# Kernel tuning notes

Measured on AMD Instinct MI355X. Metric: run time of the kernel, lower is better.

The kernel has to match this reference:

```python
import jax, jax.numpy as jnp
import numpy as np

N_NODES = 100000
N_EDGES = 800000
IN_FEATS = 128
OUT_FEATS = 128
RANK_DIM = 128
NUM_BOND_TYPES = 32


def setup_inputs() -> dict:
    key = jax.random.key(0)
    ks = jax.random.split(key, 8)
    feat = jax.random.normal(ks[0], (N_NODES, IN_FEATS), dtype=jnp.float32)
    src = jax.random.randint(ks[1], (N_EDGES,), 0, N_NODES)
    dst = jax.random.randint(ks[2], (N_EDGES,), 0, N_NODES)
    # guarantee every node has in-degree >= 1 (module forbids 0-in-degree nodes)
    dst = dst.at[:N_NODES].set(jnp.arange(N_NODES))
    edge_attr = jax.random.randint(ks[3], (N_EDGES,), 0, NUM_BOND_TYPES)
    # xavier-uniform-like params
    def xavier(k, shape):
        lim = float(np.sqrt(6.0 / (shape[0] + shape[1])))
        return jax.random.uniform(k, shape, jnp.float32, -lim, lim)
    w1 = xavier(ks[4], (IN_FEATS, OUT_FEATS))
    w2 = xavier(ks[5], (IN_FEATS + 1, RANK_DIM))
    v = xavier(ks[6], (RANK_DIM, OUT_FEATS))
    bond_emb = jax.random.normal(ks[7], (NUM_BOND_TYPES, OUT_FEATS), dtype=jnp.float32)
    return {"feat": feat, "src": src, "dst": dst, "edge_attr": edge_attr,
            "w1": w1, "w2": w2, "v": v, "bond_emb": bond_emb}


def reference(feat, src, dst, edge_attr, w1, w2, v, bond_emb):
    N = feat.shape[0]
    E = src.shape[0]
    ones_e = jnp.ones((E,), dtype=feat.dtype)
    # norm == 'both': scale source features by out_degree^{-1/2}
    out_deg = jnp.clip(jax.ops.segment_sum(ones_e, src, num_segments=N), 1.0)
    feat_src = feat * (out_deg ** -0.5)[:, None]
    # two small GEMMs on node features
    h_sum = feat_src @ w1  # [N, out]
    feat_aug = jnp.concatenate([feat_src, jnp.ones((N, 1), dtype=feat.dtype)], axis=1)
    h_prod = jnp.tanh(feat_aug @ w2)  # [N, rank]
    # edge embedding (BondEncoder)
    ew = bond_emb[edge_attr]  # [E, out]
    # u_mul_e then neighbor-wise product / sum reductions onto dst
    m_prod = h_prod[src] * ew
    m_sum = h_sum[src] * ew
    hp = jax.ops.segment_prod(m_prod, dst, num_segments=N)
    hs = jax.ops.segment_sum(m_sum, dst, num_segments=N)
    rst = hs + hp @ v
    # norm == 'both': scale result by in_degree^{-1/2}
    in_deg = jnp.clip(jax.ops.segment_sum(ones_e, dst, num_segments=N), 1.0)
    rst = rst * (in_deg ** -0.5)[:, None]
    return rst
```

## Files before the change

### kernel.cpp

```cpp
#include <hip/hip_runtime.h>

#define N_NODES 100000
#define N_EDGES 800000

typedef unsigned short u16;
typedef unsigned int u32;
typedef __attribute__((ext_vector_type(8))) short short8;
typedef __attribute__((ext_vector_type(4))) float floatx4;

#define NBUK 196
#define BSH 9
#define NBLK 512
#define NE4 (N_EDGES / 4)
#define CE 391
#define NB_PREPW 192

__device__ __forceinline__ float bflo(u32 u) {
    union { u32 i; float f; } v; v.i = u << 16; return v.f;
}
__device__ __forceinline__ float bfhi(u32 u) {
    union { u32 i; float f; } v; v.i = u & 0xFFFF0000u; return v.f;
}
__device__ __forceinline__ u16 f2bf(float f) {
    union { float f; u32 i; } v; v.f = f;
    u32 r = (v.i + 0x7FFFu + ((v.i >> 16) & 1u)) >> 16;
    return (u16)r;
}
__device__ __forceinline__ float fast_tanh(float x) {
    float e = __expf(2.0f * x);
    return 1.0f - 2.0f * __builtin_amdgcn_rcpf(e + 1.0f);
}


__global__ __launch_bounds__(256) void kA_count(const int* __restrict__ src, const int* __restrict__ dst,
                                                int* __restrict__ countsD, int* __restrict__ countsS,
                                                const float* __restrict__ w1, const float* __restrict__ w2,
                                                const float* __restrict__ v, u16* __restrict__ wvfrag) {
    __shared__ int cd[NBUK], cs[NBUK];
    if (blockIdx.x >= NBLK) {
        int idx = (blockIdx.x - NBLK) * 256 + threadIdx.x;
        if (idx < 3 * 16384) {
            int m = idx >> 14, r = idx & 16383;
            int k = r >> 7, o = r & 127;
            float val = (m == 0) ? w1[k * 128 + o] : (m == 1) ? w2[k * 128 + o] : v[k * 128 + o];
            int ot = o >> 4, ks = k >> 5, quad = (k >> 3) & 3, j = k & 7;
            int lane = (quad << 4) | (o & 15);
            wvfrag[(((m * 8 + ot) * 4 + ks) * 64 + lane) * 8 + j] = f2bf(val);
        }
        return;
    }
    for (int i = threadIdx.x; i < NBUK; i += 256) { cd[i] = 0; cs[i] = 0; }
    __syncthreads();
    int i0 = blockIdx.x * CE;
    int i1 = i0 + CE; if (i1 > NE4) i1 = NE4;
    for (int i = i0 + threadIdx.x; i < i1; i += 256) {
        int4 d4 = ((const int4*)dst)[i];
        int4 s4 = ((const int4*)src)[i];
        atomicAdd(&cd[d4.x >> BSH], 1); atomicAdd(&cd[d4.y >> BSH], 1);
        atomicAdd(&cd[d4.z >> BSH], 1); atomicAdd(&cd[d4.w >> BSH], 1);
        atomicAdd(&cs[s4.x >> BSH], 1); atomicAdd(&cs[s4.y >> BSH], 1);
        atomicAdd(&cs[s4.z >> BSH], 1); atomicAdd(&cs[s4.w >> BSH], 1);
    }
    __syncthreads();
    for (int i = threadIdx.x; i < NBUK; i += 256) {
        countsD[i * NBLK + blockIdx.x] = cd[i];
        countsS[i * NBLK + blockIdx.x] = cs[i];
    }
}


__global__ __launch_bounds__(256) void kA_scan(int* __restrict__ countsD, int* __restrict__ countsS,
                                               int* __restrict__ totD, int* __restrict__ totS) {
    __shared__ int sc[256];
    int b = blockIdx.x;
    int* cnt = (b < NBUK) ? (countsD + b * NBLK) : (countsS + (b - NBUK) * NBLK);
    int t = threadIdx.x;
    int v0 = cnt[2 * t], v1 = cnt[2 * t + 1];
    int s = v0 + v1;
    sc[t] = s; __syncthreads();
    for (int off = 1; off < 256; off <<= 1) {
        int x = (t >= off) ? sc[t - off] : 0;
        __syncthreads();
        sc[t] += x;
        __syncthreads();
    }
    int excl = sc[t] - s;
    cnt[2 * t] = excl; cnt[2 * t + 1] = excl + v0;
    if (t == 255) { if (b < NBUK) totD[b] = sc[255]; else totS[b - NBUK] = sc[255]; }
}


__global__ __launch_bounds__(256) void kA_scatter(const int* __restrict__ src, const int* __restrict__ dst,
                                                  const int* __restrict__ attr,
                                                  const int* __restrict__ countsD, const int* __restrict__ countsS,
                                                  const int* __restrict__ totD, const int* __restrict__ totS,
                                                  uint2* __restrict__ dbuf, int* __restrict__ sbuf) {
    __shared__ int curD[NBUK], curS[NBUK];
    __shared__ int sd[256], ss[256];
    int t = threadIdx.x;
    int vd = (t < NBUK) ? totD[t] : 0;
    int vs = (t < NBUK) ? totS[t] : 0;
    sd[t] = vd; ss[t] = vs; __syncthreads();
    for (int off = 1; off < 256; off <<= 1) {
        int xd = (t >= off) ? sd[t - off] : 0;
        int xs = (t >= off) ? ss[t - off] : 0;
        __syncthreads();
        sd[t] += xd; ss[t] += xs;
        __syncthreads();
    }
    if (t < NBUK) {
        curD[t] = (sd[t] - vd) + countsD[t * NBLK + blockIdx.x];
        curS[t] = (ss[t] - vs) + countsS[t * NBLK + blockIdx.x];
    }
    __syncthreads();
    int i0 = blockIdx.x * CE;
    int i1 = i0 + CE; if (i1 > NE4) i1 = NE4;
    for (int i = i0 + t; i < i1; i += 256) {
        int4 s4 = ((const int4*)src)[i];
        int4 d4 = ((const int4*)dst)[i];
        int4 a4 = ((const int4*)attr)[i];
        int p, d, s, a;
        d = d4.x; s = s4.x; a = a4.x;
        p = atomicAdd(&curD[d >> BSH], 1); dbuf[p] = make_uint2((u32)d, (u32)((s << 5) | a));
        p = atomicAdd(&curS[s >> BSH], 1); sbuf[p] = s;
        d = d4.y; s = s4.y; a = a4.y;
        p = atomicAdd(&curD[d >> BSH], 1); dbuf[p] = make_uint2((u32)d, (u32)((s << 5) | a));
        p = atomicAdd(&curS[s >> BSH], 1); sbuf[p] = s;
        d = d4.z; s = s4.z; a = a4.z;
        p = atomicAdd(&curD[d >> BSH], 1); dbuf[p] = make_uint2((u32)d, (u32)((s << 5) | a));
        p = atomicAdd(&curS[s >> BSH], 1); sbuf[p] = s;
        d = d4.w; s = s4.w; a = a4.w;
        p = atomicAdd(&curD[d >> BSH], 1); dbuf[p] = make_uint2((u32)d, (u32)((s << 5) | a));
        p = atomicAdd(&curS[s >> BSH], 1); sbuf[p] = s;
    }
}


__global__ __launch_bounds__(256) void k_build(const uint2* __restrict__ dbuf, const int* __restrict__ sbuf,
                                               const int* __restrict__ totD, const int* __restrict__ totS,
                                               int* __restrict__ csr_start, int* __restrict__ in_deg,
                                               float* __restrict__ in_scale, float* __restrict__ out_scale,
                                               int* __restrict__ csr_edge) {
    __shared__ int cnt[512];
    __shared__ int aux[512];
    __shared__ int sc[256];
    __shared__ int sbase;
    int t = threadIdx.x;
    int isS = blockIdx.x >= NBUK;
    int b = isS ? (blockIdx.x - NBUK) : blockIdx.x;
    const int* tot = isS ? totS : totD;
    if (t < 64) {
        int s = 0;
        for (int i = t; i < b; i += 64) s += tot[i];
#pragma unroll
        for (int o = 32; o > 0; o >>= 1) s += __shfl_down(s, o);
        if (t == 0) sbase = s;
    }
    for (int i = t; i < 512; i += 256) cnt[i] = 0;
    __syncthreads();
    int st = sbase, n = tot[b];
    int nb0 = b << BSH;
    if (isS) {
        for (int i = st + t; i < st + n; i += 256) atomicAdd(&cnt[sbuf[i] - nb0], 1);
        __syncthreads();
        for (int s2 = t; s2 < 512; s2 += 256) {
            int node = nb0 + s2;
            if (node < N_NODES) { int c = cnt[s2]; if (c < 1) c = 1; out_scale[node] = rsqrtf((float)c); }
        }
        return;
    }
    for (int i = st + t; i < st + n; i += 256) { uint2 r = dbuf[i]; atomicAdd(&cnt[(int)r.x - nb0], 1); }
    __syncthreads();
    int c0 = cnt[2 * t], c1 = cnt[2 * t + 1];
    int s = c0 + c1; sc[t] = s; __syncthreads();
    for (int off = 1; off < 256; off <<= 1) {
        int x = (t >= off) ? sc[t - off] : 0;
        __syncthreads();
        sc[t] += x;
        __syncthreads();
    }
    int excl = sc[t] - s;
    aux[2 * t] = excl; aux[2 * t + 1] = excl + c0;
    int na = nb0 + 2 * t, nbv = nb0 + 2 * t + 1;
    if (na < N_NODES) {
        in_deg[na] = c0; int cc = c0 < 1 ? 1 : c0;
        in_scale[na] = rsqrtf((float)cc); csr_start[na] = st + excl;
    }
    if (nbv < N_NODES) {
        in_deg[nbv] = c1; int cc = c1 < 1 ? 1 : c1;
        in_scale[nbv] = rsqrtf((float)cc); csr_start[nbv] = st + excl + c0;
    }
    __syncthreads();
    for (int i = st + t; i < st + n; i += 256) {
        uint2 r = dbuf[i];
        int pos = atomicAdd(&aux[(int)r.x - nb0], 1);
        csr_edge[st + pos] = (int)r.y;
    }
}


__global__ __launch_bounds__(256) void k_gemm(const float* __restrict__ feat,
                                              const float* __restrict__ out_scale,
                                              const u16* __restrict__ wvfrag,
                                              const float* __restrict__ w2,
                                              u16* __restrict__ hrow) {
    __shared__ u16 ldsw[32768];
    for (int i = threadIdx.x; i < 4096; i += 256)
        ((ulonglong2*)ldsw)[i] = ((const ulonglong2*)wvfrag)[i];
    __syncthreads();
    int wave = threadIdx.x >> 6, lane = threadIdx.x & 63;
    int quad = lane >> 4, l15 = lane & 15;
    const float* bias = w2 + 128 * 128;
    float bias_v[8];
#pragma unroll
    for (int ot = 0; ot < 8; ot++) bias_v[ot] = bias[ot * 16 + l15];
    const int NT = (N_NODES + 63) / 64;
    for (int tile = blockIdx.x; tile < NT; tile += gridDim.x) {
        int nb = tile * 64 + wave * 16;
        int anode = nb + l15; if (anode >= N_NODES) anode = N_NODES - 1;
        float s = out_scale[anode];
        short8 a[4];
#pragma unroll
        for (int ks = 0; ks < 4; ks++) {
            float4 f0 = *(const float4*)(feat + anode * 128 + ks * 32 + quad * 8);
            float4 f1 = *(const float4*)(feat + anode * 128 + ks * 32 + quad * 8 + 4);
            short8 av;
            av[0] = (short)f2bf(f0.x * s); av[1] = (short)f2bf(f0.y * s);
            av[2] = (short)f2bf(f0.z * s); av[3] = (short)f2bf(f0.w * s);
            av[4] = (short)f2bf(f1.x * s); av[5] = (short)f2bf(f1.y * s);
            av[6] = (short)f2bf(f1.z * s); av[7] = (short)f2bf(f1.w * s);
            a[ks] = av;
        }
#pragma unroll
        for (int ot = 0; ot < 8; ot++) {
            floatx4 accS = (floatx4){0.f, 0.f, 0.f, 0.f};
            floatx4 accP = (floatx4){0.f, 0.f, 0.f, 0.f};
#pragma unroll
            for (int ks = 0; ks < 4; ks++) {
                short8 b0 = *(const short8*)&ldsw[((ot * 4 + ks) * 64 + lane) * 8];
                short8 b1 = *(const short8*)&ldsw[16384 + ((ot * 4 + ks) * 64 + lane) * 8];
                accS = __builtin_amdgcn_mfma_f32_16x16x32_bf16(a[ks], b0, accS, 0, 0, 0);
                accP = __builtin_amdgcn_mfma_f32_16x16x32_bf16(a[ks], b1, accP, 0, 0, 0);
            }
            int o = ot * 16 + l15;
#pragma unroll
            for (int r = 0; r < 4; r++) {
                int node = nb + quad * 4 + r;
                if (node < N_NODES) {
                    u32 pv = (u32)f2bf(accS[r]) | ((u32)f2bf(fast_tanh(accP[r] + bias_v[ot])) << 16);
                    *(u32*)(hrow + node * 256 + o * 2) = pv;
                }
            }
        }
    }
}


__global__ __launch_bounds__(256, 8) void k_edge(const int* __restrict__ csr_start, const int* __restrict__ in_deg,
                                                 const int* __restrict__ csr_edge,
                                                 const u16* __restrict__ hrow,
                                                 const float* __restrict__ bond_emb,
                                                 float* __restrict__ out_hs, u16* __restrict__ hp) {
    __shared__ float ldsb[4096];
    for (int i = threadIdx.x; i < 4096; i += 256) ldsb[i] = bond_emb[i];
    __syncthreads();
    int wid = (blockIdx.x * 256 + threadIdx.x) >> 6;
    int lane = threadIdx.x & 63;
    int nwaves = (gridDim.x * 256) >> 6;
    const int NPAIR = N_NODES / 2;
    uint2 hC0 = {0, 0}, hC1 = {0, 0};
    float2 eC0 = {0.f, 0.f}, eC1 = {0.f, 0.f};
    for (int pr = wid; pr < NPAIR; pr += nwaves) {
        int n0 = pr * 2, n1 = n0 + 1;
        int st0 = csr_start[n0];
        int2 dd = *(const int2*)(in_deg + n0);
        int d0 = dd.x, d1 = dd.y;
        int st1 = st0 + d0;
        float as0 = 0.f, as1 = 0.f, ap0 = 1.f, ap1 = 1.f;
        float bs0 = 0.f, bs1 = 0.f, bp0 = 1.f, bp1 = 1.f;
        int b0 = 0, b1 = 0;
        while (b0 < d0 || b1 < d1) {
            int c0 = d0 - b0; c0 = c0 < 0 ? 0 : (c0 > 64 ? 64 : c0);
            int c1 = d1 - b1; c1 = c1 < 0 ? 0 : (c1 > 64 ? 64 : c1);
            int pkv0 = 0, pkv1 = 0;
            if (c0 > 0) { int li = lane < c0 ? lane : c0 - 1; pkv0 = csr_edge[st0 + b0 + li]; }
            if (c1 > 0) { int li = lane < c1 ? lane : c1 - 1; pkv1 = csr_edge[st1 + b1 + li]; }
            uint2 hA0 = hC0, hB0 = hC0, hA1 = hC1, hB1 = hC1;
            float2 eA0 = eC0, eB0 = eC0, eA1 = eC1, eB1 = eC1;
            if (c0 > 0) {
                int pk = __builtin_amdgcn_readlane(pkv0, 0);
                hA0 = *(const uint2*)(hrow + (pk >> 5) * 256 + 4 * lane);
                eA0 = *(const float2*)&ldsb[(pk & 31) * 128 + 2 * lane];
                if (c0 > 1) {
                    pk = __builtin_amdgcn_readlane(pkv0, 1);
                    hB0 = *(const uint2*)(hrow + (pk >> 5) * 256 + 4 * lane);
                    eB0 = *(const float2*)&ldsb[(pk & 31) * 128 + 2 * lane];
                }
            }
            if (c1 > 0) {
                int pk = __builtin_amdgcn_readlane(pkv1, 0);
                hA1 = *(const uint2*)(hrow + (pk >> 5) * 256 + 4 * lane);
                eA1 = *(const float2*)&ldsb[(pk & 31) * 128 + 2 * lane];
                if (c1 > 1) {
                    pk = __builtin_amdgcn_readlane(pkv1, 1);
                    hB1 = *(const uint2*)(hrow + (pk >> 5) * 256 + 4 * lane);
                    eB1 = *(const float2*)&ldsb[(pk & 31) * 128 + 2 * lane];
                }
            }
            int cm = c0 > c1 ? c0 : c1;
            for (int j = 0; j < cm; j++) {
                int jn = j + 2;
                if (jn < c0) {
                    int pk = __builtin_amdgcn_readlane(pkv0, jn);
                    hC0 = *(const uint2*)(hrow + (pk >> 5) * 256 + 4 * lane);
                    eC0 = *(const float2*)&ldsb[(pk & 31) * 128 + 2 * lane];
                }
                if (jn < c1) {
                    int pk = __builtin_amdgcn_readlane(pkv1, jn);
                    hC1 = *(const uint2*)(hrow + (pk >> 5) * 256 + 4 * lane);
                    eC1 = *(const float2*)&ldsb[(pk & 31) * 128 + 2 * lane];
                }
                if (j < c0) {
                    as0 += bflo(hA0.x) * eA0.x;
                    ap0 *= bfhi(hA0.x) * eA0.x;
                    as1 += bflo(hA0.y) * eA0.y;
                    ap1 *= bfhi(hA0.y) * eA0.y;
                    hA0 = hB0; eA0 = eB0; hB0 = hC0; eB0 = eC0;
                }
                if (j < c1) {
                    bs0 += bflo(hA1.x) * eA1.x;
                    bp0 *= bfhi(hA1.x) * eA1.x;
                    bs1 += bflo(hA1.y) * eA1.y;
                    bp1 *= bfhi(hA1.y) * eA1.y;
                    hA1 = hB1; eA1 = eB1; hB1 = hC1; eB1 = eC1;
                }
            }
            b0 += 64; b1 += 64;
        }
        float2 sv0; sv0.x = as0; sv0.y = as1;
        float2 sv1; sv1.x = bs0; sv1.y = bs1;
        *(float2*)(out_hs + n0 * 128 + 2 * lane) = sv0;
        *(float2*)(out_hs + n1 * 128 + 2 * lane) = sv1;
        *(u32*)(hp + n0 * 128 + 2 * lane) = ((u32)f2bf(ap1) << 16) | (u32)f2bf(ap0);
        *(u32*)(hp + n1 * 128 + 2 * lane) = ((u32)f2bf(bp1) << 16) | (u32)f2bf(bp0);
    }
}


__global__ __launch_bounds__(256) void k_final(const u16* __restrict__ hp,
                                               const u16* __restrict__ vfrag,
                                               const float* __restrict__ in_scale,
                                               float* __restrict__ out) {
    __shared__ u16 ldsw[16384];
    for (int i = threadIdx.x; i < 2048; i += 256)
        ((ulonglong2*)ldsw)[i] = ((const ulonglong2*)vfrag)[i];
    __syncthreads();
    int wave = threadIdx.x >> 6, lane = threadIdx.x & 63;
    int quad = lane >> 4, l15 = lane & 15;
    const int NT = (N_NODES + 63) / 64;
    for (int tile = blockIdx.x; tile < NT; tile += gridDim.x) {
        int nb = tile * 64 + wave * 16;
        int anode = nb + l15; if (anode >= N_NODES) anode = N_NODES - 1;
        short8 a[4];
#pragma unroll
        for (int ks = 0; ks < 4; ks++)
            a[ks] = *(const short8*)(hp + anode * 128 + ks * 32 + quad * 8);
#pragma unroll
        for (int ot = 0; ot < 8; ot++) {
            floatx4 acc = (floatx4){0.f, 0.f, 0.f, 0.f};
#pragma unroll
            for (int ks = 0; ks < 4; ks++) {
                short8 b = *(const short8*)&ldsw[((ot * 4 + ks) * 64 + lane) * 8];
                acc = __builtin_amdgcn_mfma_f32_16x16x32_bf16(a[ks], b, acc, 0, 0, 0);
            }
            int o = ot * 16 + l15;
#pragma unroll
            for (int r = 0; r < 4; r++) {
                int node = nb + quad * 4 + r;
                if (node < N_NODES) {
                    float scl = in_scale[node];
                    float hsv = out[node * 128 + o];
                    out[node * 128 + o] = (acc[r] + hsv) * scl;
                }
            }
        }
    }
}

extern "C" void kernel_launch(void* const* d_in, const int* in_sizes, int n_in,
                              void* d_out, int out_size, void* d_ws, size_t ws_size,
                              hipStream_t stream) {
    const float* feat = (const float*)d_in[0];
    const int* src = (const int*)d_in[1];
    const int* dst = (const int*)d_in[2];
    const int* attr = (const int*)d_in[3];
    const float* w1 = (const float*)d_in[4];
    const float* w2 = (const float*)d_in[5];
    const float* v = (const float*)d_in[6];
    const float* bond = (const float*)d_in[7];
    float* out = (float*)d_out;

    char* ws = (char*)d_ws;
    size_t off = 0;
    auto alloc = [&](size_t bytes) -> char* {
        char* p = ws + off; off += (bytes + 255) & ~(size_t)255; return p;
    };
    int* countsD   = (int*)alloc((size_t)NBUK * NBLK * 4);
    int* countsS   = (int*)alloc((size_t)NBUK * NBLK * 4);
    int* totD      = (int*)alloc((size_t)NBUK * 4);
    int* totS      = (int*)alloc((size_t)NBUK * 4);
    uint2* dbuf    = (uint2*)alloc((size_t)N_EDGES * 8);
    int* sbuf      = (int*)alloc((size_t)N_EDGES * 4);
    int* csr_start = (int*)alloc((size_t)N_NODES * 4);
    int* in_deg    = (int*)alloc((size_t)N_NODES * 4);
    float* out_scale = (float*)alloc((size_t)N_NODES * 4);
    float* in_scale  = (float*)alloc((size_t)N_NODES * 4);
    int* csr_edge  = (int*)alloc((size_t)N_EDGES * 4);
    u16* wvfrag = (u16*)alloc((size_t)3 * 16384 * 2);
    u16* hrow   = (u16*)alloc((size_t)N_NODES * 256 * 2);
    u16* hp     = (u16*)alloc((size_t)N_NODES * 128 * 2);

    (void)in_sizes; (void)n_in; (void)out_size; (void)ws_size;

    kA_count<<<NBLK + NB_PREPW, 256, 0, stream>>>(src, dst, countsD, countsS, w1, w2, v, wvfrag);
    kA_scan<<<2 * NBUK, 256, 0, stream>>>(countsD, countsS, totD, totS);
    kA_scatter<<<NBLK, 256, 0, stream>>>(src, dst, attr, countsD, countsS, totD, totS, dbuf, sbuf);
    k_build<<<2 * NBUK, 256, 0, stream>>>(dbuf, sbuf, totD, totS,
                                          csr_start, in_deg, in_scale, out_scale, csr_edge);
    k_gemm<<<512, 256, 0, stream>>>(feat, out_scale, wvfrag, w2, hrow);
    k_edge<<<2048, 256, 0, stream>>>(csr_start, in_deg, csr_edge, hrow, bond, out, hp);
    k_final<<<1280, 256, 0, stream>>>(hp, wvfrag + 2 * 16384, in_scale, out);
}
```

Measured before the change: 295.4 us.

## Balance edge work per wave, deepen gather prefetch, drop LDS staging

k_edge now gives each wave a contiguous range of node pairs holding an equal share of edges, found by binary search over csr_start, replacing the strided pair assignment. It also deepens the gather software pipeline from 2 to 3 edges in flight and reads bond embeddings straight from global memory (cache) instead of staging them in LDS. k_gemm drops its LDS weight staging and persistent tile loop, launching one block per 64-node tile and reading weight fragments directly from global memory. Together these aim to cut load imbalance, LDS setup and sync cost, and exposed gather latency, at the cost of more VGPRs and more cache traffic for the weights.

```diff
diff --git a/kernel.cpp b/kernel.cpp
--- a/kernel.cpp
+++ b/kernel.cpp
@@ -204,73 +204,78 @@
                                               const u16* __restrict__ wvfrag,
                                               const float* __restrict__ w2,
                                               u16* __restrict__ hrow) {
-    __shared__ u16 ldsw[32768];
-    for (int i = threadIdx.x; i < 4096; i += 256)
-        ((ulonglong2*)ldsw)[i] = ((const ulonglong2*)wvfrag)[i];
-    __syncthreads();
     int wave = threadIdx.x >> 6, lane = threadIdx.x & 63;
     int quad = lane >> 4, l15 = lane & 15;
     const float* bias = w2 + 128 * 128;
     float bias_v[8];
 #pragma unroll
     for (int ot = 0; ot < 8; ot++) bias_v[ot] = bias[ot * 16 + l15];
-    const int NT = (N_NODES + 63) / 64;
-    for (int tile = blockIdx.x; tile < NT; tile += gridDim.x) {
-        int nb = tile * 64 + wave * 16;
-        int anode = nb + l15; if (anode >= N_NODES) anode = N_NODES - 1;
-        float s = out_scale[anode];
-        short8 a[4];
+    const short8* wv = (const short8*)wvfrag;
+    int nb = blockIdx.x * 64 + wave * 16;
+    int anode = nb + l15; if (anode >= N_NODES) anode = N_NODES - 1;
+    float s = out_scale[anode];
+    short8 a[4];
+#pragma unroll
+    for (int ks = 0; ks < 4; ks++) {
+        float4 f0 = *(const float4*)(feat + anode * 128 + ks * 32 + quad * 8);
+        float4 f1 = *(const float4*)(feat + anode * 128 + ks * 32 + quad * 8 + 4);
+        short8 av;
+        av[0] = (short)f2bf(f0.x * s); av[1] = (short)f2bf(f0.y * s);
+        av[2] = (short)f2bf(f0.z * s); av[3] = (short)f2bf(f0.w * s);
+        av[4] = (short)f2bf(f1.x * s); av[5] = (short)f2bf(f1.y * s);
+        av[6] = (short)f2bf(f1.z * s); av[7] = (short)f2bf(f1.w * s);
+        a[ks] = av;
+    }
+#pragma unroll
+    for (int ot = 0; ot < 8; ot++) {
+        floatx4 accS = (floatx4){0.f, 0.f, 0.f, 0.f};
+        floatx4 accP = (floatx4){0.f, 0.f, 0.f, 0.f};
 #pragma unroll
         for (int ks = 0; ks < 4; ks++) {
-            float4 f0 = *(const float4*)(feat + anode * 128 + ks * 32 + quad * 8);
-            float4 f1 = *(const float4*)(feat + anode * 128 + ks * 32 + quad * 8 + 4);
-            short8 av;
-            av[0] = (short)f2bf(f0.x * s); av[1] = (short)f2bf(f0.y * s);
-            av[2] = (short)f2bf(f0.z * s); av[3] = (short)f2bf(f0.w * s);
-            av[4] = (short)f2bf(f1.x * s); av[5] = (short)f2bf(f1.y * s);
-            av[6] = (short)f2bf(f1.z * s); av[7] = (short)f2bf(f1.w * s);
-            a[ks] = av;
-        }
-#pragma unroll
-        for (int ot = 0; ot < 8; ot++) {
-            floatx4 accS = (floatx4){0.f, 0.f, 0.f, 0.f};
-            floatx4 accP = (floatx4){0.f, 0.f, 0.f, 0.f};
-#pragma unroll
-            for (int ks = 0; ks < 4; ks++) {
-                short8 b0 = *(const short8*)&ldsw[((ot * 4 + ks) * 64 + lane) * 8];
-                short8 b1 = *(const short8*)&ldsw[16384 + ((ot * 4 + ks) * 64 + lane) * 8];
-                accS = __builtin_amdgcn_mfma_f32_16x16x32_bf16(a[ks], b0, accS, 0, 0, 0);
-                accP = __builtin_amdgcn_mfma_f32_16x16x32_bf16(a[ks], b1, accP, 0, 0, 0);
-            }
-            int o = ot * 16 + l15;
-#pragma unroll
-            for (int r = 0; r < 4; r++) {
-                int node = nb + quad * 4 + r;
-                if (node < N_NODES) {
-                    u32 pv = (u32)f2bf(accS[r]) | ((u32)f2bf(fast_tanh(accP[r] + bias_v[ot])) << 16);
-                    *(u32*)(hrow + node * 256 + o * 2) = pv;
-                }
-            }
-        }
-    }
-}
-
+            short8 b0 = wv[(ot * 4 + ks) * 64 + lane];
+            short8 b1 = wv[((8 + ot) * 4 + ks) * 64 + lane];
+            accS = __builtin_amdgcn_mfma_f32_16x16x32_bf16(a[ks], b0, accS, 0, 0, 0);
+            accP = __builtin_amdgcn_mfma_f32_16x16x32_bf16(a[ks], b1, accP, 0, 0, 0);
+        }
+        int o = ot * 16 + l15;
+#pragma unroll
+        for (int r = 0; r < 4; r++) {
+            int node = nb + quad * 4 + r;
+            if (node < N_NODES) {
+                u32 pv = (u32)f2bf(accS[r]) | ((u32)f2bf(fast_tanh(accP[r] + bias_v[ot])) << 16);
+                *(u32*)(hrow + node * 256 + o * 2) = pv;
+            }
+        }
+    }
+}
+
+
+__device__ __forceinline__ int pair_lb(const int* __restrict__ csr_start, long long tgt) {
+    const int NPAIR = N_NODES / 2;
+    int lo = 0, hi = NPAIR;
+    while (lo < hi) {
+        int mid = (lo + hi + 1) >> 1;
+        int v = (mid == NPAIR) ? N_EDGES : csr_start[2 * mid];
+        if (v <= tgt) lo = mid; else hi = mid - 1;
+    }
+    return lo;
+}
 
 __global__ __launch_bounds__(256, 8) void k_edge(const int* __restrict__ csr_start, const int* __restrict__ in_deg,
                                                  const int* __restrict__ csr_edge,
                                                  const u16* __restrict__ hrow,
                                                  const float* __restrict__ bond_emb,
                                                  float* __restrict__ out_hs, u16* __restrict__ hp) {
-    __shared__ float ldsb[4096];
-    for (int i = threadIdx.x; i < 4096; i += 256) ldsb[i] = bond_emb[i];
-    __syncthreads();
     int wid = (blockIdx.x * 256 + threadIdx.x) >> 6;
     int lane = threadIdx.x & 63;
     int nwaves = (gridDim.x * 256) >> 6;
-    const int NPAIR = N_NODES / 2;
-    uint2 hC0 = {0, 0}, hC1 = {0, 0};
-    float2 eC0 = {0.f, 0.f}, eC1 = {0.f, 0.f};
-    for (int pr = wid; pr < NPAIR; pr += nwaves) {
+    long long t0 = ((long long)wid * N_EDGES) / nwaves;
+    long long t1 = ((long long)(wid + 1) * N_EDGES) / nwaves;
+    int p0 = pair_lb(csr_start, t0);
+    int p1 = pair_lb(csr_start, t1);
+    uint2 hD0 = {0, 0}, hD1 = {0, 0};
+    float2 eD0 = {0.f, 0.f}, eD1 = {0.f, 0.f};
+    for (int pr = p0; pr < p1; pr++) {
         int n0 = pr * 2, n1 = n0 + 1;
         int st0 = csr_start[n0];
         int2 dd = *(const int2*)(in_deg + n0);
@@ -285,54 +290,64 @@
             int pkv0 = 0, pkv1 = 0;
             if (c0 > 0) { int li = lane < c0 ? lane : c0 - 1; pkv0 = csr_edge[st0 + b0 + li]; }
             if (c1 > 0) { int li = lane < c1 ? lane : c1 - 1; pkv1 = csr_edge[st1 + b1 + li]; }
-            uint2 hA0 = hC0, hB0 = hC0, hA1 = hC1, hB1 = hC1;
-            float2 eA0 = eC0, eB0 = eC0, eA1 = eC1, eB1 = eC1;
+            uint2 hA0 = hD0, hB0 = hD0, hC0 = hD0, hA1 = hD1, hB1 = hD1, hC1 = hD1;
+            float2 eA0 = eD0, eB0 = eD0, eC0 = eD0, eA1 = eD1, eB1 = eD1, eC1 = eD1;
             if (c0 > 0) {
                 int pk = __builtin_amdgcn_readlane(pkv0, 0);
                 hA0 = *(const uint2*)(hrow + (pk >> 5) * 256 + 4 * lane);
-                eA0 = *(const float2*)&ldsb[(pk & 31) * 128 + 2 * lane];
+                eA0 = *(const float2*)(bond_emb + (pk & 31) * 128 + 2 * lane);
                 if (c0 > 1) {
                     pk = __builtin_amdgcn_readlane(pkv0, 1);
                     hB0 = *(const uint2*)(hrow + (pk >> 5) * 256 + 4 * lane);
-                    eB0 = *(const float2*)&ldsb[(pk & 31) * 128 + 2 * lane];
+                    eB0 = *(const float2*)(bond_emb + (pk & 31) * 128 + 2 * lane);
+                    if (c0 > 2) {
+                        pk = __builtin_amdgcn_readlane(pkv0, 2);
+                        hC0 = *(const uint2*)(hrow + (pk >> 5) * 256 + 4 * lane);
+                        eC0 = *(const float2*)(bond_emb + (pk & 31) * 128 + 2 * lane);
+                    }
                 }
             }
             if (c1 > 0) {
                 int pk = __builtin_amdgcn_readlane(pkv1, 0);
                 hA1 = *(const uint2*)(hrow + (pk >> 5) * 256 + 4 * lane);
-                eA1 = *(const float2*)&ldsb[(pk & 31) * 128 + 2 * lane];
+                eA1 = *(const float2*)(bond_emb + (pk & 31) * 128 + 2 * lane);
                 if (c1 > 1) {
                     pk = __builtin_amdgcn_readlane(pkv1, 1);
                     hB1 = *(const uint2*)(hrow + (pk >> 5) * 256 + 4 * lane);
-                    eB1 = *(const float2*)&ldsb[(pk & 31) * 128 + 2 * lane];
+                    eB1 = *(const float2*)(bond_emb + (pk & 31) * 128 + 2 * lane);
+                    if (c1 > 2) {
+                        pk = __builtin_amdgcn_readlane(pkv1, 2);
+                        hC1 = *(const uint2*)(hrow + (pk >> 5) * 256 + 4 * lane);
+                        eC1 = *(const float2*)(bond_emb + (pk & 31) * 128 + 2 * lane);
+                    }
                 }
             }
             int cm = c0 > c1 ? c0 : c1;
             for (int j = 0; j < cm; j++) {
-                int jn = j + 2;
+                int jn = j + 3;
                 if (jn < c0) {
                     int pk = __builtin_amdgcn_readlane(pkv0, jn);
-                    hC0 = *(const uint2*)(hrow + (pk >> 5) * 256 + 4 * lane);
-                    eC0 = *(const float2*)&ldsb[(pk & 31) * 128 + 2 * lane];
+                    hD0 = *(const uint2*)(hrow + (pk >> 5) * 256 + 4 * lane);
+                    eD0 = *(const float2*)(bond_emb + (pk & 31) * 128 + 2 * lane);
                 }
                 if (jn < c1) {
                     int pk = __builtin_amdgcn_readlane(pkv1, jn);
-                    hC1 = *(const uint2*)(hrow + (pk >> 5) * 256 + 4 * lane);
-                    eC1 = *(const float2*)&ldsb[(pk & 31) * 128 + 2 * lane];
+                    hD1 = *(const uint2*)(hrow + (pk >> 5) * 256 + 4 * lane);
+                    eD1 = *(const float2*)(bond_emb + (pk & 31) * 128 + 2 * lane);
                 }
                 if (j < c0) {
                     as0 += bflo(hA0.x) * eA0.x;
                     ap0 *= bfhi(hA0.x) * eA0.x;
                     as1 += bflo(hA0.y) * eA0.y;
                     ap1 *= bfhi(hA0.y) * eA0.y;
-                    hA0 = hB0; eA0 = eB0; hB0 = hC0; eB0 = eC0;
+                    hA0 = hB0; eA0 = eB0; hB0 = hC0; eB0 = eC0; hC0 = hD0; eC0 = eD0;
                 }
                 if (j < c1) {
                     bs0 += bflo(hA1.x) * eA1.x;
                     bp0 *= bfhi(hA1.x) * eA1.x;
                     bs1 += bflo(hA1.y) * eA1.y;
                     bp1 *= bfhi(hA1.y) * eA1.y;
-                    hA1 = hB1; eA1 = eB1; hB1 = hC1; eB1 = eC1;
+                    hA1 = hB1; eA1 = eB1; hB1 = hC1; eB1 = eC1; hC1 = hD1; eC1 = eD1;
                 }
             }
             b0 += 64; b1 += 64;
@@ -427,7 +442,7 @@
     kA_scatter<<<NBLK, 256, 0, stream>>>(src, dst, attr, countsD, countsS, totD, totS, dbuf, sbuf);
     k_build<<<2 * NBUK, 256, 0, stream>>>(dbuf, sbuf, totD, totS,
                                           csr_start, in_deg, in_scale, out_scale, csr_edge);
-    k_gemm<<<512, 256, 0, stream>>>(feat, out_scale, wvfrag, w2, hrow);
+    k_gemm<<<(N_NODES + 63) / 64, 256, 0, stream>>>(feat, out_scale, wvfrag, w2, hrow);
     k_edge<<<2048, 256, 0, stream>>>(csr_start, in_deg, csr_edge, hrow, bond, out, hp);
     k_final<<<1280, 256, 0, stream>>>(hp, wvfrag + 2 * 16384, in_scale, out);
 }
```

Result: slower. 302.5 us (+2.4%).
